# Optimization experiments

Measured on AMD Instinct MI355X. Metric: run time of the kernel, lower is better.

## Reference

```python
import jax, jax.numpy as jnp
import numpy as np

N = 100000
E = 1600000
IN_CH = 128
EDGE_CH = 16
HID = 128
OUT = 4
EPS = 1e-12  # F.normalize eps


def l2_normalize(x):
    # matches torch.nn.functional.normalize(x, p=2, dim=1)
    norm = jnp.sqrt(jnp.sum(x * x, axis=1, keepdims=True))
    return x / jnp.maximum(norm, EPS)


def sage_conv(x, row, col, edge_attr, W, b, n_nodes):
    # gather source node feats, concat edge feats: [E, in+edge]
    m = jnp.concatenate([x[row], edge_attr], axis=1)
    m = l2_normalize(m)
    # scatter-mean by destination node
    s = jax.ops.segment_sum(m, col, num_segments=n_nodes)
    cnt = jax.ops.segment_sum(jnp.ones((m.shape[0],), m.dtype), col, num_segments=n_nodes)
    agg = s / jnp.maximum(cnt, 1.0)[:, None]
    out = agg @ W + b
    return l2_normalize(out)


def setup_inputs() -> dict:
    key = jax.random.key(0)
    ks = jax.random.split(key, 7)
    x = jax.random.normal(ks[0], (N, IN_CH), dtype=jnp.float32)
    edge_index = jax.random.randint(ks[1], (2, E), 0, N, dtype=jnp.int64)
    edge_attr = jax.random.normal(ks[2], (E, EDGE_CH), dtype=jnp.float32)
    W1 = jax.random.normal(ks[3], (IN_CH + EDGE_CH, HID), dtype=jnp.float32) / np.sqrt(IN_CH + EDGE_CH)
    b1 = jnp.zeros((HID,), dtype=jnp.float32)
    W2 = jax.random.normal(ks[4], (HID + EDGE_CH, OUT), dtype=jnp.float32) / np.sqrt(HID + EDGE_CH)
    b2 = jnp.zeros((OUT,), dtype=jnp.float32)
    return {"x": x, "edge_index": edge_index, "edge_attr": edge_attr,
            "W1": W1, "b1": b1, "W2": W2, "b2": b2}


def reference(x, edge_index, edge_attr, W1, b1, W2, b2):
    row, col = edge_index[0], edge_index[1]
    h = sage_conv(x, row, col, edge_attr, W1, b1, N)
    h = jax.nn.relu(h)  # dropout is identity in eval mode
    h = sage_conv(h, row, col, edge_attr, W2, b2, N)
    return jax.nn.sigmoid(h)
```

## Files before the change

kernel.cpp:

```cpp
#include <hip/hip_runtime.h>
#include <hip/hip_fp16.h>
#include <math.h>

#define N_NODES 100000
#define N_EDGES 1600000
#define CHUNK 1024
#define NCHUNKS ((N_NODES + CHUNK - 1) / CHUNK)

union H8 { uint4 u; __half2 h[4]; };

__device__ __forceinline__ float red32(float v) {
    #pragma unroll
    for (int m = 16; m >= 1; m >>= 1) v += __shfl_xor(v, m, 64);
    return v;
}

__global__ __launch_bounds__(256) void hist(const int* __restrict__ col,
                                            int* __restrict__ cnt) {
    int e = blockIdx.x * blockDim.x + threadIdx.x;
    if (e >= N_EDGES) return;
    atomicAdd(&cnt[col[e]], 1);
}

__global__ void scan_part(const int* __restrict__ cnt, int* __restrict__ psum) {
    __shared__ int sd[CHUNK];
    int i = blockIdx.x * CHUNK + threadIdx.x;
    sd[threadIdx.x] = (i < N_NODES) ? cnt[i] : 0;
    __syncthreads();
    for (int s = CHUNK / 2; s > 0; s >>= 1) {
        if (threadIdx.x < s) sd[threadIdx.x] += sd[threadIdx.x + s];
        __syncthreads();
    }
    if (threadIdx.x == 0) psum[blockIdx.x] = sd[0];
}

__global__ void scan_top(const int* __restrict__ psum, int* __restrict__ coff,
                         int* __restrict__ off) {
    if (blockIdx.x == 0 && threadIdx.x == 0) {
        int run = 0;
        for (int i = 0; i < NCHUNKS; ++i) { coff[i] = run; run += psum[i]; }
        off[N_NODES] = N_EDGES;
    }
}

__global__ void scan_apply(const int* __restrict__ cnt, const int* __restrict__ coff,
                           int* __restrict__ off, int* __restrict__ head) {
    __shared__ int sd[CHUNK];
    int i = blockIdx.x * CHUNK + threadIdx.x;
    int v = (i < N_NODES) ? cnt[i] : 0;
    sd[threadIdx.x] = v;
    __syncthreads();
    for (int s = 1; s < CHUNK; s <<= 1) {
        int t = (threadIdx.x >= s) ? sd[threadIdx.x - s] : 0;
        __syncthreads();
        sd[threadIdx.x] += t;
        __syncthreads();
    }
    if (i < N_NODES) {
        int excl = coff[blockIdx.x] + sd[threadIdx.x] - v;
        off[i] = excl;
        head[i] = excl;
    }
}

__global__ __launch_bounds__(256) void gemm_y1h(const float* __restrict__ x,
                                                const float* __restrict__ W1,
                                                __half* __restrict__ y1h,
                                                float* __restrict__ nx) {
    __shared__ float xs[64][129];
    int r0 = blockIdx.x * 64;
    int t = threadIdx.x;
    for (int i = t; i < 64 * 32; i += 256) {
        int rr = i >> 5, c4 = (i & 31) * 4;
        int gr = r0 + rr;
        float4 v = (gr < N_NODES) ? *(const float4*)(x + (size_t)gr * 128 + c4)
                                  : make_float4(0.f, 0.f, 0.f, 0.f);
        xs[rr][c4] = v.x; xs[rr][c4 + 1] = v.y; xs[rr][c4 + 2] = v.z; xs[rr][c4 + 3] = v.w;
    }
    __syncthreads();
    {
        int rr = t >> 2, q = t & 3;
        float s = 0.f;
        #pragma unroll
        for (int k = 0; k < 32; ++k) { float v = xs[rr][q * 32 + k]; s += v * v; }
        s += __shfl_xor(s, 1, 64);
        s += __shfl_xor(s, 2, 64);
        if (q == 0 && r0 + rr < N_NODES) nx[r0 + rr] = s;
    }
    int tx = t & 31, ty = t >> 5;
    float4 acc[8];
    #pragma unroll
    for (int i = 0; i < 8; ++i) acc[i] = make_float4(0.f, 0.f, 0.f, 0.f);
    #pragma unroll 4
    for (int k = 0; k < 128; ++k) {
        float4 wv = *(const float4*)(W1 + (size_t)k * 128 + tx * 4);
        #pragma unroll
        for (int i = 0; i < 8; ++i) {
            float xv = xs[ty * 8 + i][k];
            acc[i].x += xv * wv.x; acc[i].y += xv * wv.y;
            acc[i].z += xv * wv.z; acc[i].w += xv * wv.w;
        }
    }
    #pragma unroll
    for (int i = 0; i < 8; ++i) {
        int rr = r0 + ty * 8 + i;
        if (rr < N_NODES) {
            H8 pk;
            pk.h[0] = __float22half2_rn(make_float2(acc[i].x, acc[i].y));
            pk.h[1] = __float22half2_rn(make_float2(acc[i].z, acc[i].w));
            *(uint2*)(y1h + (size_t)rr * 128 + tx * 4) = make_uint2(pk.u.x, pk.u.y);
        }
    }
}

__global__ __launch_bounds__(256) void scatter_e(
        const int* __restrict__ row, const int* __restrict__ col,
        const float* __restrict__ nx, const float* __restrict__ ea,
        int* __restrict__ head, int4* __restrict__ csrM) {
    int e = blockIdx.x * blockDim.x + threadIdx.x;
    if (e >= N_EDGES) return;
    const float4* p = (const float4*)(ea + (size_t)e * 16);
    float4 q0 = p[0], q1 = p[1], q2 = p[2], q3 = p[3];
    float s = q0.x*q0.x + q0.y*q0.y + q0.z*q0.z + q0.w*q0.w
            + q1.x*q1.x + q1.y*q1.y + q1.z*q1.z + q1.w*q1.w
            + q2.x*q2.x + q2.y*q2.y + q2.z*q2.z + q2.w*q2.w
            + q3.x*q3.x + q3.y*q3.y + q3.z*q3.z + q3.w*q3.w;
    int r = row[e];
    int c = col[e];
    float w1 = rsqrtf(fmaxf(nx[r] + s, 1e-24f));
    int pp = atomicAdd(&head[c], 1);
    int4 mt; mt.x = r; mt.y = __float_as_int(w1); mt.z = e; mt.w = __float_as_int(s);
    csrM[pp] = mt;
}

__global__ __launch_bounds__(256) void layer1(
        const __half* __restrict__ y1h, const float* __restrict__ ea,
        const int4* __restrict__ csrM, const int* __restrict__ off,
        const float* __restrict__ W1, const float* __restrict__ b1,
        const float* __restrict__ W2, float* __restrict__ hn) {
    __shared__ int4  smeta[4][64];
    __shared__ float strans[4][144];
    int wv = threadIdx.x >> 6;
    int node = (blockIdx.x << 2) | wv;
    int lane = threadIdx.x & 63;
    if (node >= N_NODES) return;
    int s = off[node], e = off[node + 1];
    int deg = e - s;
    int m = (deg < 64) ? deg : 64;
    if (lane < m) smeta[wv][lane] = csrM[s + lane];
    asm volatile("s_waitcnt lgkmcnt(0)" ::: "memory");

    int e4 = lane >> 4;
    int c8 = lane & 15;
    float4 a0 = make_float4(0,0,0,0), a1 = a0;
    float4 sea = a0;

    #pragma unroll 2
    for (int t = 0; t < m; t += 4) {
        int idx = t + e4;
        bool val = idx < m;
        int4 mt = smeta[wv][val ? idx : 0];
        int r = mt.x;
        float w = val ? __int_as_float(mt.y) : 0.f;
        H8 pk; pk.u = *(const uint4*)(y1h + (size_t)r * 128 + c8 * 8);
        float2 f0 = __half22float2(pk.h[0]);
        float2 f1 = __half22float2(pk.h[1]);
        float2 f2 = __half22float2(pk.h[2]);
        float2 f3 = __half22float2(pk.h[3]);
        a0.x += f0.x * w; a0.y += f0.y * w; a0.z += f1.x * w; a0.w += f1.y * w;
        a1.x += f2.x * w; a1.y += f2.y * w; a1.z += f3.x * w; a1.w += f3.y * w;
        if (c8 < 4) {
            float4 ev = *(const float4*)(ea + (size_t)mt.z * 16 + c8 * 4);
            sea.x += ev.x * w; sea.y += ev.y * w;
            sea.z += ev.z * w; sea.w += ev.w * w;
        }
    }
    for (int t = 64 + e4; t < deg; t += 4) {
        int4 mt = csrM[s + t];
        int r = mt.x;
        float w = __int_as_float(mt.y);
        H8 pk; pk.u = *(const uint4*)(y1h + (size_t)r * 128 + c8 * 8);
        float2 f0 = __half22float2(pk.h[0]);
        float2 f1 = __half22float2(pk.h[1]);
        float2 f2 = __half22float2(pk.h[2]);
        float2 f3 = __half22float2(pk.h[3]);
        a0.x += f0.x * w; a0.y += f0.y * w; a0.z += f1.x * w; a0.w += f1.y * w;
        a1.x += f2.x * w; a1.y += f2.y * w; a1.z += f3.x * w; a1.w += f3.y * w;
        if (c8 < 4) {
            float4 ev = *(const float4*)(ea + (size_t)mt.z * 16 + c8 * 4);
            sea.x += ev.x * w; sea.y += ev.y * w;
            sea.z += ev.z * w; sea.w += ev.w * w;
        }
    }
    #pragma unroll
    for (int mm = 16; mm <= 32; mm <<= 1) {
        a0.x += __shfl_xor(a0.x, mm, 64); a0.y += __shfl_xor(a0.y, mm, 64);
        a0.z += __shfl_xor(a0.z, mm, 64); a0.w += __shfl_xor(a0.w, mm, 64);
        a1.x += __shfl_xor(a1.x, mm, 64); a1.y += __shfl_xor(a1.y, mm, 64);
        a1.z += __shfl_xor(a1.z, mm, 64); a1.w += __shfl_xor(a1.w, mm, 64);
        sea.x += __shfl_xor(sea.x, mm, 64); sea.y += __shfl_xor(sea.y, mm, 64);
        sea.z += __shfl_xor(sea.z, mm, 64); sea.w += __shfl_xor(sea.w, mm, 64);
    }
    if (e4 == 0) {
        *(float4*)&strans[wv][c8 * 8]     = a0;
        *(float4*)&strans[wv][c8 * 8 + 4] = a1;
        if (c8 < 4) *(float4*)&strans[wv][128 + c8 * 4] = sea;
    }
    asm volatile("s_waitcnt lgkmcnt(0)" ::: "memory");

    int c = lane & 31;
    float ic = 1.0f / fmaxf((float)deg, 1.0f);
    float4 av = *(const float4*)&strans[wv][c * 4];
    float4 b1v = *(const float4*)(b1 + c * 4);
    float4 o;
    o.x = av.x * ic + b1v.x; o.y = av.y * ic + b1v.y;
    o.z = av.z * ic + b1v.z; o.w = av.w * ic + b1v.w;
    #pragma unroll
    for (int k = 0; k < 16; ++k) {
        float sk = strans[wv][128 + k] * ic;
        float4 wv4 = *((const float4*)(W1 + (size_t)(128 + k) * 128) + c);
        o.x += sk * wv4.x; o.y += sk * wv4.y; o.z += sk * wv4.z; o.w += sk * wv4.w;
    }
    float ss    = o.x*o.x + o.y*o.y + o.z*o.z + o.w*o.w;
    float sspos = (o.x > 0.f ? o.x*o.x : 0.f) + (o.y > 0.f ? o.y*o.y : 0.f)
                + (o.z > 0.f ? o.z*o.z : 0.f) + (o.w > 0.f ? o.w*o.w : 0.f);
    ss = red32(ss);
    sspos = red32(sspos);
    float inv = rsqrtf(fmaxf(ss, 1e-24f));
    float4 h4;
    h4.x = fmaxf(o.x * inv, 0.f); h4.y = fmaxf(o.y * inv, 0.f);
    h4.z = fmaxf(o.z * inv, 0.f); h4.w = fmaxf(o.w * inv, 0.f);
    float nhv = sspos * inv * inv;
    float4 w0 = *(const float4*)(W2 + (size_t)(4*c + 0) * 4);
    float4 w1 = *(const float4*)(W2 + (size_t)(4*c + 1) * 4);
    float4 w2 = *(const float4*)(W2 + (size_t)(4*c + 2) * 4);
    float4 w3 = *(const float4*)(W2 + (size_t)(4*c + 3) * 4);
    float4 p;
    p.x = h4.x*w0.x + h4.y*w1.x + h4.z*w2.x + h4.w*w3.x;
    p.y = h4.x*w0.y + h4.y*w1.y + h4.z*w2.y + h4.w*w3.y;
    p.z = h4.x*w0.z + h4.y*w1.z + h4.z*w2.z + h4.w*w3.z;
    p.w = h4.x*w0.w + h4.y*w1.w + h4.z*w2.w + h4.w*w3.w;
    p.x = red32(p.x); p.y = red32(p.y); p.z = red32(p.z); p.w = red32(p.w);
    if (lane == 0) {
        *(float4*)(hn + (size_t)node * 8) = p;
        hn[(size_t)node * 8 + 4] = nhv;
    }
}

__global__ __launch_bounds__(256) void layer2(
        const int4* __restrict__ csrM, const float* __restrict__ ea,
        const float* __restrict__ hn, const int* __restrict__ off,
        const float* __restrict__ W2, const float* __restrict__ b2,
        float* __restrict__ out) {
    __shared__ int4 smeta[4][64];
    int wv = threadIdx.x >> 6;
    int node = (blockIdx.x << 2) | wv;
    int lane = threadIdx.x & 63;
    if (node >= N_NODES) return;
    int s = off[node], e = off[node + 1];
    int deg = e - s;
    int m = (deg < 64) ? deg : 64;
    if (lane < m) smeta[wv][lane] = csrM[s + lane];
    asm volatile("s_waitcnt lgkmcnt(0)" ::: "memory");
    int e16 = lane >> 2, q = lane & 3;
    float4 w2r0 = *(const float4*)(W2 + (size_t)(128 + q * 4 + 0) * 4);
    float4 w2r1 = *(const float4*)(W2 + (size_t)(128 + q * 4 + 1) * 4);
    float4 w2r2 = *(const float4*)(W2 + (size_t)(128 + q * 4 + 2) * 4);
    float4 w2r3 = *(const float4*)(W2 + (size_t)(128 + q * 4 + 3) * 4);

    float4 acc = make_float4(0.f, 0.f, 0.f, 0.f);
    float4 sea = make_float4(0.f, 0.f, 0.f, 0.f);
    for (int t = e16; t < m; t += 16) {
        int4 mt = smeta[wv][t];
        int r = mt.x;
        float sq = __int_as_float(mt.w);
        float nh = hn[(size_t)r * 8 + 4];
        float w = rsqrtf(fmaxf(nh + sq, 1e-24f));
        float4 yh = *(const float4*)(hn + (size_t)r * 8);
        float4 ev = *(const float4*)(ea + (size_t)mt.z * 16 + q * 4);
        acc.x += w * yh.x; acc.y += w * yh.y; acc.z += w * yh.z; acc.w += w * yh.w;
        sea.x += w * ev.x; sea.y += w * ev.y; sea.z += w * ev.z; sea.w += w * ev.w;
    }
    for (int t = 64 + e16; t < deg; t += 16) {
        int4 mt = csrM[s + t];
        int r = mt.x;
        float sq = __int_as_float(mt.w);
        float nh = hn[(size_t)r * 8 + 4];
        float w = rsqrtf(fmaxf(nh + sq, 1e-24f));
        float4 yh = *(const float4*)(hn + (size_t)r * 8);
        float4 ev = *(const float4*)(ea + (size_t)mt.z * 16 + q * 4);
        acc.x += w * yh.x; acc.y += w * yh.y; acc.z += w * yh.z; acc.w += w * yh.w;
        sea.x += w * ev.x; sea.y += w * ev.y; sea.z += w * ev.z; sea.w += w * ev.w;
    }
    #pragma unroll
    for (int mm = 4; mm <= 32; mm <<= 1) {
        acc.x += __shfl_xor(acc.x, mm, 64); acc.y += __shfl_xor(acc.y, mm, 64);
        acc.z += __shfl_xor(acc.z, mm, 64); acc.w += __shfl_xor(acc.w, mm, 64);
        sea.x += __shfl_xor(sea.x, mm, 64); sea.y += __shfl_xor(sea.y, mm, 64);
        sea.z += __shfl_xor(sea.z, mm, 64); sea.w += __shfl_xor(sea.w, mm, 64);
    }
    float4 pv;
    pv.x = sea.x*w2r0.x + sea.y*w2r1.x + sea.z*w2r2.x + sea.w*w2r3.x;
    pv.y = sea.x*w2r0.y + sea.y*w2r1.y + sea.z*w2r2.y + sea.w*w2r3.y;
    pv.z = sea.x*w2r0.z + sea.y*w2r1.z + sea.z*w2r2.z + sea.w*w2r3.z;
    pv.w = sea.x*w2r0.w + sea.y*w2r1.w + sea.z*w2r2.w + sea.w*w2r3.w;
    #pragma unroll
    for (int mm = 1; mm <= 2; mm <<= 1) {
        pv.x += __shfl_xor(pv.x, mm, 64); pv.y += __shfl_xor(pv.y, mm, 64);
        pv.z += __shfl_xor(pv.z, mm, 64); pv.w += __shfl_xor(pv.w, mm, 64);
    }
    if (lane == 0) {
        float ic = 1.0f / fmaxf((float)deg, 1.0f);
        float4 o;
        o.x = (acc.x + pv.x) * ic + b2[0];
        o.y = (acc.y + pv.y) * ic + b2[1];
        o.z = (acc.z + pv.z) * ic + b2[2];
        o.w = (acc.w + pv.w) * ic + b2[3];
        float ss = o.x*o.x + o.y*o.y + o.z*o.z + o.w*o.w;
        float inv = rsqrtf(fmaxf(ss, 1e-24f));
        float4 res;
        res.x = 1.0f / (1.0f + expf(-(o.x * inv)));
        res.y = 1.0f / (1.0f + expf(-(o.y * inv)));
        res.z = 1.0f / (1.0f + expf(-(o.z * inv)));
        res.w = 1.0f / (1.0f + expf(-(o.w * inv)));
        *(float4*)(out + (size_t)node * 4) = res;
    }
}

extern "C" void kernel_launch(void* const* d_in, const int* in_sizes, int n_in,
                              void* d_out, int out_size, void* d_ws, size_t ws_size,
                              hipStream_t stream) {
    const float* x   = (const float*)d_in[0];
    const int*   ei  = (const int*)d_in[1];
    const float* ea  = (const float*)d_in[2];
    const float* W1  = (const float*)d_in[3];
    const float* b1  = (const float*)d_in[4];
    const float* W2  = (const float*)d_in[5];
    const float* b2  = (const float*)d_in[6];
    const int* row = ei;
    const int* col = ei + N_EDGES;
    float* out = (float*)d_out;

    char* ws = (char*)d_ws;
    size_t o = 0;
    auto carve = [&](size_t bytes) { char* p = ws + o; o = (o + bytes + 255) & ~(size_t)255; return p; };
    __half* y1h    = (__half*)carve((size_t)N_NODES * 128 * 2);
    int4*   csrM   = (int4*)carve((size_t)N_EDGES * 16);
    int*    cnt    = (int*)carve((size_t)N_NODES * 4);
    int*    off    = (int*)carve((size_t)(N_NODES + 1) * 4);
    int*    head   = (int*)carve((size_t)N_NODES * 4);
    float*  nx     = (float*)carve((size_t)N_NODES * 4);
    float*  hn     = (float*)carve((size_t)N_NODES * 8 * 4);
    int*    psum   = (int*)carve((size_t)NCHUNKS * 4);
    int*    coff   = (int*)carve((size_t)NCHUNKS * 4);
    (void)ws_size; (void)in_sizes; (void)n_in; (void)out_size;

    hipMemsetAsync(cnt, 0, (size_t)N_NODES * 4, stream);

    dim3 b256(256);
    hist<<<(N_EDGES + 255) / 256, b256, 0, stream>>>(col, cnt);
    gemm_y1h<<<(N_NODES + 63) / 64, b256, 0, stream>>>(x, W1, y1h, nx);

    scan_part<<<NCHUNKS, CHUNK, 0, stream>>>(cnt, psum);
    scan_top<<<1, 64, 0, stream>>>(psum, coff, off);
    scan_apply<<<NCHUNKS, CHUNK, 0, stream>>>(cnt, coff, off, head);
    scatter_e<<<(N_EDGES + 255) / 256, b256, 0, stream>>>(row, col, nx, ea, head, csrM);

    layer1<<<(N_NODES + 3) / 4, b256, 0, stream>>>(y1h, ea, csrM, off, W1, b1, W2, hn);
    layer2<<<(N_NODES + 3) / 4, b256, 0, stream>>>(csrM, ea, hn, off, W2, b2, out);
}
```

Before: 386.1 us.

## Shrink CSR metadata to (row, edge) pairs and recompute edge norms in consumers

The scatter kernel no longer reads edge attributes or computes the first-layer normalization weight. It now writes only an 8-byte (source, edge id) pair per edge instead of a 16-byte record, which halves CSR metadata traffic and removes a full pass over edge_attr from scatter. Both layer kernels now compute the edge squared norm from the edge attributes they already load, reduce it with lane shuffles, and in layer1 also load nx[r] per edge to form the weight. The cost is extra shuffles and ALU work per edge, plus an extra nx gather in layer1.

```diff
diff --git a/kernel.cpp b/kernel.cpp
--- a/kernel.cpp
+++ b/kernel.cpp
@@ -115,30 +115,22 @@
 
 __global__ __launch_bounds__(256) void scatter_e(
         const int* __restrict__ row, const int* __restrict__ col,
-        const float* __restrict__ nx, const float* __restrict__ ea,
-        int* __restrict__ head, int4* __restrict__ csrM) {
+        int* __restrict__ head, uint2* __restrict__ csrM) {
     int e = blockIdx.x * blockDim.x + threadIdx.x;
     if (e >= N_EDGES) return;
-    const float4* p = (const float4*)(ea + (size_t)e * 16);
-    float4 q0 = p[0], q1 = p[1], q2 = p[2], q3 = p[3];
-    float s = q0.x*q0.x + q0.y*q0.y + q0.z*q0.z + q0.w*q0.w
-            + q1.x*q1.x + q1.y*q1.y + q1.z*q1.z + q1.w*q1.w
-            + q2.x*q2.x + q2.y*q2.y + q2.z*q2.z + q2.w*q2.w
-            + q3.x*q3.x + q3.y*q3.y + q3.z*q3.z + q3.w*q3.w;
     int r = row[e];
     int c = col[e];
-    float w1 = rsqrtf(fmaxf(nx[r] + s, 1e-24f));
     int pp = atomicAdd(&head[c], 1);
-    int4 mt; mt.x = r; mt.y = __float_as_int(w1); mt.z = e; mt.w = __float_as_int(s);
-    csrM[pp] = mt;
+    csrM[pp] = make_uint2((unsigned)r, (unsigned)e);
 }
 
 __global__ __launch_bounds__(256) void layer1(
         const __half* __restrict__ y1h, const float* __restrict__ ea,
-        const int4* __restrict__ csrM, const int* __restrict__ off,
+        const float* __restrict__ nx,
+        const uint2* __restrict__ csrM, const int* __restrict__ off,
         const float* __restrict__ W1, const float* __restrict__ b1,
         const float* __restrict__ W2, float* __restrict__ hn) {
-    __shared__ int4  smeta[4][64];
+    __shared__ uint2 smeta[4][64];
     __shared__ float strans[4][144];
     int wv = threadIdx.x >> 6;
     int node = (blockIdx.x << 2) | wv;
@@ -152,6 +144,7 @@
 
     int e4 = lane >> 4;
     int c8 = lane & 15;
+    int bsrc = lane & 0x30;
     float4 a0 = make_float4(0,0,0,0), a1 = a0;
     float4 sea = a0;
 
@@ -159,38 +152,51 @@
     for (int t = 0; t < m; t += 4) {
         int idx = t + e4;
         bool val = idx < m;
-        int4 mt = smeta[wv][val ? idx : 0];
-        int r = mt.x;
-        float w = val ? __int_as_float(mt.y) : 0.f;
+        uint2 mt = smeta[wv][val ? idx : 0];
+        int r = (int)mt.x;
         H8 pk; pk.u = *(const uint4*)(y1h + (size_t)r * 128 + c8 * 8);
+        float4 ev = make_float4(0.f, 0.f, 0.f, 0.f);
+        float sq = 0.f;
+        if (c8 < 4) {
+            ev = *(const float4*)(ea + (size_t)mt.y * 16 + c8 * 4);
+            sq = ev.x*ev.x + ev.y*ev.y + ev.z*ev.z + ev.w*ev.w;
+        }
+        sq += __shfl_xor(sq, 1, 64);
+        sq += __shfl_xor(sq, 2, 64);
+        float wp = (c8 == 0) ? rsqrtf(fmaxf(nx[r] + sq, 1e-24f)) : 0.f;
+        float w = __shfl(wp, bsrc, 64);
+        if (!val) w = 0.f;
         float2 f0 = __half22float2(pk.h[0]);
         float2 f1 = __half22float2(pk.h[1]);
         float2 f2 = __half22float2(pk.h[2]);
         float2 f3 = __half22float2(pk.h[3]);
         a0.x += f0.x * w; a0.y += f0.y * w; a0.z += f1.x * w; a0.w += f1.y * w;
         a1.x += f2.x * w; a1.y += f2.y * w; a1.z += f3.x * w; a1.w += f3.y * w;
+        sea.x += ev.x * w; sea.y += ev.y * w;
+        sea.z += ev.z * w; sea.w += ev.w * w;
+    }
+    for (int t = 64 + e4; t < deg; t += 4) {
+        uint2 mt = csrM[s + t];
+        int r = (int)mt.x;
+        H8 pk; pk.u = *(const uint4*)(y1h + (size_t)r * 128 + c8 * 8);
+        float4 ev = make_float4(0.f, 0.f, 0.f, 0.f);
+        float sq = 0.f;
         if (c8 < 4) {
-            float4 ev = *(const float4*)(ea + (size_t)mt.z * 16 + c8 * 4);
-            sea.x += ev.x * w; sea.y += ev.y * w;
-            sea.z += ev.z * w; sea.w += ev.w * w;
+            ev = *(const float4*)(ea + (size_t)mt.y * 16 + c8 * 4);
+            sq = ev.x*ev.x + ev.y*ev.y + ev.z*ev.z + ev.w*ev.w;
         }
-    }
-    for (int t = 64 + e4; t < deg; t += 4) {
-        int4 mt = csrM[s + t];
-        int r = mt.x;
-        float w = __int_as_float(mt.y);
-        H8 pk; pk.u = *(const uint4*)(y1h + (size_t)r * 128 + c8 * 8);
+        sq += __shfl_xor(sq, 1, 64);
+        sq += __shfl_xor(sq, 2, 64);
+        float wp = (c8 == 0) ? rsqrtf(fmaxf(nx[r] + sq, 1e-24f)) : 0.f;
+        float w = __shfl(wp, bsrc, 64);
         float2 f0 = __half22float2(pk.h[0]);
         float2 f1 = __half22float2(pk.h[1]);
         float2 f2 = __half22float2(pk.h[2]);
         float2 f3 = __half22float2(pk.h[3]);
         a0.x += f0.x * w; a0.y += f0.y * w; a0.z += f1.x * w; a0.w += f1.y * w;
         a1.x += f2.x * w; a1.y += f2.y * w; a1.z += f3.x * w; a1.w += f3.y * w;
-        if (c8 < 4) {
-            float4 ev = *(const float4*)(ea + (size_t)mt.z * 16 + c8 * 4);
-            sea.x += ev.x * w; sea.y += ev.y * w;
-            sea.z += ev.z * w; sea.w += ev.w * w;
-        }
+        sea.x += ev.x * w; sea.y += ev.y * w;
+        sea.z += ev.z * w; sea.w += ev.w * w;
     }
     #pragma unroll
     for (int mm = 16; mm <= 32; mm <<= 1) {
@@ -248,11 +254,11 @@
 }
 
 __global__ __launch_bounds__(256) void layer2(
-        const int4* __restrict__ csrM, const float* __restrict__ ea,
+        const uint2* __restrict__ csrM, const float* __restrict__ ea,
         const float* __restrict__ hn, const int* __restrict__ off,
         const float* __restrict__ W2, const float* __restrict__ b2,
         float* __restrict__ out) {
-    __shared__ int4 smeta[4][64];
+    __shared__ uint2 smeta[4][64];
     int wv = threadIdx.x >> 6;
     int node = (blockIdx.x << 2) | wv;
     int lane = threadIdx.x & 63;
@@ -271,24 +277,28 @@
     float4 acc = make_float4(0.f, 0.f, 0.f, 0.f);
     float4 sea = make_float4(0.f, 0.f, 0.f, 0.f);
     for (int t = e16; t < m; t += 16) {
-        int4 mt = smeta[wv][t];
-        int r = mt.x;
-        float sq = __int_as_float(mt.w);
+        uint2 mt = smeta[wv][t];
+        int r = (int)mt.x;
+        float4 ev = *(const float4*)(ea + (size_t)mt.y * 16 + q * 4);
+        float sq = ev.x*ev.x + ev.y*ev.y + ev.z*ev.z + ev.w*ev.w;
+        sq += __shfl_xor(sq, 1, 64);
+        sq += __shfl_xor(sq, 2, 64);
         float nh = hn[(size_t)r * 8 + 4];
         float w = rsqrtf(fmaxf(nh + sq, 1e-24f));
         float4 yh = *(const float4*)(hn + (size_t)r * 8);
-        float4 ev = *(const float4*)(ea + (size_t)mt.z * 16 + q * 4);
         acc.x += w * yh.x; acc.y += w * yh.y; acc.z += w * yh.z; acc.w += w * yh.w;
         sea.x += w * ev.x; sea.y += w * ev.y; sea.z += w * ev.z; sea.w += w * ev.w;
     }
     for (int t = 64 + e16; t < deg; t += 16) {
-        int4 mt = csrM[s + t];
-        int r = mt.x;
-        float sq = __int_as_float(mt.w);
+        uint2 mt = csrM[s + t];
+        int r = (int)mt.x;
+        float4 ev = *(const float4*)(ea + (size_t)mt.y * 16 + q * 4);
+        float sq = ev.x*ev.x + ev.y*ev.y + ev.z*ev.z + ev.w*ev.w;
+        sq += __shfl_xor(sq, 1, 64);
+        sq += __shfl_xor(sq, 2, 64);
         float nh = hn[(size_t)r * 8 + 4];
         float w = rsqrtf(fmaxf(nh + sq, 1e-24f));
         float4 yh = *(const float4*)(hn + (size_t)r * 8);
-        float4 ev = *(const float4*)(ea + (size_t)mt.z * 16 + q * 4);
         acc.x += w * yh.x; acc.y += w * yh.y; acc.z += w * yh.z; acc.w += w * yh.w;
         sea.x += w * ev.x; sea.y += w * ev.y; sea.z += w * ev.z; sea.w += w * ev.w;
     }
@@ -345,7 +355,7 @@
     size_t o = 0;
     auto carve = [&](size_t bytes) { char* p = ws + o; o = (o + bytes + 255) & ~(size_t)255; return p; };
     __half* y1h    = (__half*)carve((size_t)N_NODES * 128 * 2);
-    int4*   csrM   = (int4*)carve((size_t)N_EDGES * 16);
+    uint2*  csrM   = (uint2*)carve((size_t)N_EDGES * 8);
     int*    cnt    = (int*)carve((size_t)N_NODES * 4);
     int*    off    = (int*)carve((size_t)(N_NODES + 1) * 4);
     int*    head   = (int*)carve((size_t)N_NODES * 4);
@@ -364,8 +374,9 @@
     scan_part<<<NCHUNKS, CHUNK, 0, stream>>>(cnt, psum);
     scan_top<<<1, 64, 0, stream>>>(psum, coff, off);
     scan_apply<<<NCHUNKS, CHUNK, 0, stream>>>(cnt, coff, off, head);
-    scatter_e<<<(N_EDGES + 255) / 256, b256, 0, stream>>>(row, col, nx, ea, head, csrM);
-
-    layer1<<<(N_NODES + 3) / 4, b256, 0, stream>>>(y1h, ea, csrM, off, W1, b1, W2, hn);
+    scatter_e<<<(N_EDGES + 255) / 256, b256, 0, stream>>>(row, col, head, csrM);
+
+    layer1<<<(N_NODES + 3) / 4, b256, 0, stream>>>(y1h, ea, nx, csrM, off,
+                                                   W1, b1, W2, hn);
     layer2<<<(N_NODES + 3) / 4, b256, 0, stream>>>(csrM, ea, hn, off, W2, b2, out);
 }
```

Result: slower. 456.2 us (+18.2%).
